# Performance work log

Measured on AMD Instinct MI355X. Metric: run time of the kernel, lower is better.

Reference implementation:

```python
import jax, jax.numpy as jnp
import numpy as np


def _knn_idx(query, ref, k):
    # query [B,Q,F], ref [B,M,F] -> indices [B,Q,k] of k nearest refs (L2)
    d2 = (jnp.sum(query * query, -1)[..., None]
          - 2.0 * jnp.einsum('bqf,bmf->bqm', query, ref)
          + jnp.sum(ref * ref, -1)[:, None, :])
    _, idx = jax.lax.top_k(-d2, k)
    return idx


def _gather(pts, idx):
    # pts [B,M,F], idx [B,Q,k] -> [B,Q,k,F]
    return jax.vmap(lambda p, i: p[i])(pts, idx)


def _mlp(h, W1, b1, W2, b2):
    # pointwise 1x1-conv MLP: Conv1d(k=1) == per-point matmul
    return jax.nn.relu(h @ W1 + b1) @ W2 + b2


def setup_inputs() -> dict:
    key = jax.random.key(0)
    ks = jax.random.split(key, 12)
    B, N, S1, S2 = 8, 16384, 512, 128

    def p(k, shape, fan):
        return jax.random.normal(k, shape, jnp.float32) / np.float32(np.sqrt(fan))

    return {
        'x': jax.random.normal(ks[0], (B, N, 3), jnp.float32),
        'sample_idx1': jnp.sort(jax.random.randint(ks[1], (S1,), 0, N)),
        'sample_idx2': jnp.sort(jax.random.randint(ks[2], (S2,), 0, S1)),
        'sa1_W1': p(ks[3], (3, 64), 3), 'sa1_b1': jnp.zeros((64,), jnp.float32),
        'sa1_W2': p(ks[4], (64, 64), 64), 'sa1_b2': jnp.zeros((64,), jnp.float32),
        'sa2_W1': p(ks[5], (64, 128), 64), 'sa2_b1': jnp.zeros((128,), jnp.float32),
        'sa2_W2': p(ks[6], (128, 128), 128), 'sa2_b2': jnp.zeros((128,), jnp.float32),
        'fp1_W1': p(ks[7], (192, 64), 192), 'fp1_b1': jnp.zeros((64,), jnp.float32),
        'fp1_W2': p(ks[8], (64, 64), 64), 'fp1_b2': jnp.zeros((64,), jnp.float32),
        'fp2_W1': p(ks[9], (67, 32), 67), 'fp2_b1': jnp.zeros((32,), jnp.float32),
        'fp2_W2': p(ks[10], (32, 32), 32), 'fp2_b2': jnp.zeros((32,), jnp.float32),
        'fc_W': p(ks[11], (32, 2), 32), 'fc_b': jnp.zeros((2,), jnp.float32),
    }


def reference(x, sample_idx1, sample_idx2,
              sa1_W1, sa1_b1, sa1_W2, sa1_b2,
              sa2_W1, sa2_b1, sa2_W2, sa2_b2,
              fp1_W1, fp1_b1, fp1_W2, fp1_b2,
              fp2_W1, fp2_b1, fp2_W2, fp2_b2,
              fc_W, fc_b):
    G = 32  # group_points
    # --- SetAbstraction 1 (KNN grouping in xyz space) ---
    samp1 = x[:, sample_idx1]                                  # [B,S1,3]
    g1 = _gather(x, _knn_idx(samp1, x, G))                     # [B,S1,G,3]
    feat1 = jnp.max(_mlp(g1, sa1_W1, sa1_b1, sa1_W2, sa1_b2), axis=2)   # [B,S1,64]
    # --- SetAbstraction 2 (point cloud = SA1 features, as in source) ---
    samp2 = feat1[:, sample_idx2]                              # [B,S2,64]
    g2 = _gather(feat1, _knn_idx(samp2, feat1, G))             # [B,S2,G,64]
    feat2 = jnp.max(_mlp(g2, sa2_W1, sa2_b1, sa2_W2, sa2_b2), axis=2)   # [B,S2,128]
    coords2 = samp1[:, sample_idx2]                            # [B,S2,3]
    # --- FeaturePropagation 1: interpolate feat2 onto the S1 points (3-NN mean) ---
    interp1 = jnp.mean(_gather(feat2, _knn_idx(samp1, coords2, 3)), axis=2)  # [B,S1,128]
    h1 = _mlp(jnp.concatenate([feat1, interp1], -1), fp1_W1, fp1_b1, fp1_W2, fp1_b2)  # [B,S1,64]
    # --- FeaturePropagation 2: interpolate onto all N points ---
    interp2 = jnp.mean(_gather(h1, _knn_idx(x, samp1, 3)), axis=2)           # [B,N,64]
    h2 = _mlp(jnp.concatenate([x, interp2], -1), fp2_W1, fp2_b1, fp2_W2, fp2_b2)      # [B,N,32]
    return jax.nn.sigmoid(h2 @ fc_W + fc_b)                    # [B,N,2]
```

## Files before the change

### kernel.cpp

```cpp
#include <hip/hip_runtime.h>
#include <hip/hip_bf16.h>

#define NB   8
#define NPTS 16384
#define NS1  512
#define NS2  128
#define KNN  32
#define FINF 3.402823466e+38f
#define NINF_BITS ((int)0xFF800000)

__device__ __forceinline__ void topk32f(float key, int idx, int lane,
                                        float& lkey, int& lidx, float& tau,
                                        unsigned long long mask) {
  const bool is16 = (lane == 16);
  while (mask) {
    const int src = (int)(__ffsll((long long)mask) - 1);
    mask &= mask - 1;
    const float ck = __int_as_float(
        __builtin_amdgcn_readlane(__float_as_int(key), src));
    if (ck < tau) {
      const int ci = __builtin_amdgcn_readlane(idx, src);
      const int upk0 = __builtin_amdgcn_update_dpp(
          NINF_BITS, __float_as_int(lkey), 0x111, 0xf, 0xf, false);
      const int upi0 = __builtin_amdgcn_update_dpp(
          0, lidx, 0x111, 0xf, 0xf, false);
      const int pk = __builtin_amdgcn_readlane(__float_as_int(lkey), 15);
      const int pi = __builtin_amdgcn_readlane(lidx, 15);
      const float up  = __int_as_float(is16 ? pk : upk0);
      const int   upi = is16 ? pi : upi0;
      const bool keep  = (lkey <= ck);
      const bool useup = (up > ck);
      const float nk = keep ? lkey : (useup ? up : ck);
      const int   ni = keep ? lidx : (useup ? upi : ci);
      if (lane < 32) { lkey = nk; lidx = ni; }
      tau = __int_as_float(__builtin_amdgcn_readlane(__float_as_int(lkey), 31));
    }
  }
}

__device__ __forceinline__ void merge3(float& d0, int& j0, float& d1, int& j1,
                                       float& d2, int& j2, int xm) {
  float e0 = __shfl_xor(d0, xm), e1 = __shfl_xor(d1, xm), e2 = __shfl_xor(d2, xm);
  int   f0 = __shfl_xor(j0, xm), f1 = __shfl_xor(j1, xm), f2 = __shfl_xor(j2, xm);
  float a0 = d0, a1 = d1, a2 = d2;
  int   b0 = j0, b1 = j1, b2 = j2;
  float od0, od1, od2; int oj0, oj1, oj2;
  #pragma unroll
  for (int r = 0; r < 3; ++r) {
    bool ta = (a0 < e0) || (a0 == e0 && b0 < f0);
    float sd = ta ? a0 : e0; int sj = ta ? b0 : f0;
    a0 = ta ? a1 : a0;  b0 = ta ? b1 : b0;
    a1 = ta ? a2 : a1;  b1 = ta ? b2 : b1;
    a2 = ta ? FINF : a2;
    e0 = ta ? e0 : e1;  f0 = ta ? f0 : f1;
    e1 = ta ? e1 : e2;  f1 = ta ? f1 : f2;
    e2 = ta ? e2 : FINF;
    if (r == 0) { od0 = sd; oj0 = sj; }
    else if (r == 1) { od1 = sd; oj1 = sj; }
    else { od2 = sd; oj2 = sj; }
  }
  d0 = od0; j0 = oj0; d1 = od1; j1 = oj1; d2 = od2; j2 = oj2;
}

extern "C" __global__ void __launch_bounds__(256)
prep_kernel(const float* __restrict__ x, float4* __restrict__ xr) {
  const int i = blockIdx.x * 256 + threadIdx.x;
  const float rx = x[i*3+0], ry = x[i*3+1], rz = x[i*3+2];
  xr[i] = make_float4(rx, ry, rz, rx*rx + ry*ry + rz*rz);
}

#define PROCF(rr, jbase)                                                      \
  {                                                                           \
    const float d = (Q.w - 2.0f*(Q.x*rr.x + Q.y*rr.y + Q.z*rr.z)) + rr.w;     \
    const unsigned long long mask = __ballot(d < tau);                        \
    if (mask) topk32f(d, (jbase) + lane, lane, lkey, lidx, tau, mask);        \
  }

extern "C" __global__ void __launch_bounds__(256)
knn1_kernel(const float4* __restrict__ xr, const int* __restrict__ sidx1,
            int* __restrict__ idx1) {
  const int w = threadIdx.x >> 6, lane = threadIdx.x & 63;
  const int gq = blockIdx.x * 4 + w;
  const int b = gq >> 9, q = gq & (NS1 - 1);
  const float4* xb = xr + (size_t)b * NPTS;
  const float4 Q = xb[sidx1[q]];
  float lkey = FINF, tau = FINF;
  int lidx = 0;
  float4 r0 = xb[0*64+lane], r1 = xb[1*64+lane], r2 = xb[2*64+lane], r3 = xb[3*64+lane];
  float4 r4 = xb[4*64+lane], r5 = xb[5*64+lane], r6 = xb[6*64+lane], r7 = xb[7*64+lane];
  for (int t = 0; t < 256; t += 8) {
    PROCF(r0, (t+0)*64);  r0 = xb[((t+ 8)&255)*64 + lane];
    PROCF(r1, (t+1)*64);  r1 = xb[((t+ 9)&255)*64 + lane];
    PROCF(r2, (t+2)*64);  r2 = xb[((t+10)&255)*64 + lane];
    PROCF(r3, (t+3)*64);  r3 = xb[((t+11)&255)*64 + lane];
    PROCF(r4, (t+4)*64);  r4 = xb[((t+12)&255)*64 + lane];
    PROCF(r5, (t+5)*64);  r5 = xb[((t+13)&255)*64 + lane];
    PROCF(r6, (t+6)*64);  r6 = xb[((t+14)&255)*64 + lane];
    PROCF(r7, (t+7)*64);  r7 = xb[((t+15)&255)*64 + lane];
  }
  if (lane < 32) idx1[gq*KNN + lane] = lidx;
}

extern "C" __global__ void __launch_bounds__(256)
mlp1_kernel(const float* __restrict__ x, const int* __restrict__ sidx1,
            const int* __restrict__ idx1,
            const float* __restrict__ W1, const float* __restrict__ b1,
            const float* __restrict__ W2, const float* __restrict__ b2,
            float* __restrict__ feat1, float* __restrict__ rr1,
            float* __restrict__ samp1) {
  __shared__ float P[32][3];
  __shared__ float H[32][64];
  __shared__ float PM[4][64];
  const int tid = threadIdx.x;
  const int gq = blockIdx.x;
  const int b = gq >> 9, q = gq & (NS1-1);
  const float* xb = x + (size_t)b * NPTS * 3;
  const int* nb = idx1 + gq * KNN;
  if (tid < 96) { int n = tid/3, d = tid - n*3; P[n][d] = xb[nb[n]*3 + d]; }
  __syncthreads();
  #pragma unroll
  for (int i = 0; i < 8; ++i) {
    int e = tid + 256*i, n = e >> 6, c = e & 63;
    float h = b1[c] + P[n][0]*W1[c] + P[n][1]*W1[64+c] + P[n][2]*W1[128+c];
    H[n][c] = fmaxf(h, 0.0f);
  }
  __syncthreads();
  const int g = tid >> 6, c = tid & 63;
  float acc[8];
  #pragma unroll
  for (int k = 0; k < 8; ++k) acc[k] = 0.0f;
  for (int j = 0; j < 64; j += 4) {
    float w0 = W2[j*64+c], w1 = W2[(j+1)*64+c], w2 = W2[(j+2)*64+c], w3 = W2[(j+3)*64+c];
    #pragma unroll
    for (int k = 0; k < 8; ++k) {
      float4 h4 = *(const float4*)&H[g*8+k][j];
      acc[k] = fmaf(h4.w, w3, fmaf(h4.z, w2, fmaf(h4.y, w1, fmaf(h4.x, w0, acc[k]))));
    }
  }
  float m = acc[0];
  #pragma unroll
  for (int k = 1; k < 8; ++k) m = fmaxf(m, acc[k]);
  PM[g][c] = m;
  __syncthreads();
  if (tid < 64) {
    float v = fmaxf(fmaxf(PM[0][tid], PM[1][tid]), fmaxf(PM[2][tid], PM[3][tid])) + b2[tid];
    feat1[(size_t)gq*64 + tid] = v;
    float s = v*v;
    #pragma unroll
    for (int off = 32; off; off >>= 1) s += __shfl_xor(s, off);
    if (tid == 0) rr1[gq] = s;
  } else if (tid < 67) {
    int d = tid - 64;
    samp1[(size_t)gq*3 + d] = xb[sidx1[q]*3 + d];
  }
}

extern "C" __global__ void __launch_bounds__(256)
knn2_kernel(const float* __restrict__ feat1, const float* __restrict__ rr1,
            const int* __restrict__ sidx2, int* __restrict__ idx2) {
  __shared__ float qrow[4][64];
  const int w = threadIdx.x >> 6, lane = threadIdx.x & 63;
  const int gq = blockIdx.x*4 + w;
  const int b = gq >> 7, q = gq & (NS2-1);
  const int sq = sidx2[q];
  const float* f1b = feat1 + (size_t)b * NS1 * 64;
  const float* rrb = rr1 + b * NS1;
  qrow[w][lane] = f1b[sq*64 + lane];
  __syncthreads();
  const float qq = rrb[sq];
  float lkey = FINF, tau = FINF;
  int lidx = 0;
  for (int t = 0; t < NS1/64; ++t) {
    const int j = t*64 + lane;
    const float* rrow = f1b + j*64;
    float dot = 0.0f;
    #pragma unroll
    for (int f = 0; f < 64; f += 4) {
      float4 r4 = *(const float4*)(rrow + f);
      dot = fmaf(qrow[w][f+3], r4.w, fmaf(qrow[w][f+2], r4.z,
            fmaf(qrow[w][f+1], r4.y, fmaf(qrow[w][f+0], r4.x, dot))));
    }
    const float d = (qq - 2.0f*dot) + rrb[j];
    const unsigned long long mask = __ballot(d < tau);
    if (mask) topk32f(d, j, lane, lkey, lidx, tau, mask);
  }
  if (lane < 32) idx2[gq*KNN + lane] = lidx;
}

extern "C" __global__ void __launch_bounds__(256)
mlp2_kernel(const float* __restrict__ feat1, const int* __restrict__ idx2,
            const float* __restrict__ W1, const float* __restrict__ b1,
            const float* __restrict__ W2, const float* __restrict__ b2,
            float* __restrict__ feat2) {
  __shared__ float Gm[32][64];
  __shared__ float H[32][128];
  __shared__ float PM[2][128];
  const int tid = threadIdx.x;
  const int gq = blockIdx.x;
  const int b = gq >> 7;
  const float* f1b = feat1 + (size_t)b * NS1 * 64;
  const int* nb = idx2 + gq * KNN;
  #pragma unroll
  for (int i = 0; i < 8; ++i) {
    int e = tid + 256*i, n = e >> 6, f = e & 63;
    Gm[n][f] = f1b[nb[n]*64 + f];
  }
  __syncthreads();
  #pragma unroll
  for (int i = 0; i < 16; ++i) {
    int e = tid + 256*i, n = e >> 7, c = e & 127;
    float h = b1[c];
    for (int f = 0; f < 64; f += 4) {
      float4 g4 = *(const float4*)&Gm[n][f];
      h = fmaf(g4.x, W1[f*128+c], h);
      h = fmaf(g4.y, W1[(f+1)*128+c], h);
      h = fmaf(g4.z, W1[(f+2)*128+c], h);
      h = fmaf(g4.w, W1[(f+3)*128+c], h);
    }
    H[n][c] = fmaxf(h, 0.0f);
  }
  __syncthreads();
  const int g = tid >> 7, c = tid & 127;
  float acc[16];
  #pragma unroll
  for (int k = 0; k < 16; ++k) acc[k] = 0.0f;
  for (int j = 0; j < 128; j += 4) {
    float w0 = W2[j*128+c], w1 = W2[(j+1)*128+c], w2 = W2[(j+2)*128+c], w3 = W2[(j+3)*128+c];
    #pragma unroll
    for (int k = 0; k < 16; ++k) {
      float4 h4 = *(const float4*)&H[g*16+k][j];
      acc[k] = fmaf(h4.w, w3, fmaf(h4.z, w2, fmaf(h4.y, w1, fmaf(h4.x, w0, acc[k]))));
    }
  }
  float m = acc[0];
  #pragma unroll
  for (int k = 1; k < 16; ++k) m = fmaxf(m, acc[k]);
  PM[g][c] = m;
  __syncthreads();
  if (tid < 128) feat2[(size_t)gq*128 + tid] = fmaxf(PM[0][tid], PM[1][tid]) + b2[tid];
}

extern "C" __global__ void __launch_bounds__(256)
fp1_kernel(const float* __restrict__ samp1, const int* __restrict__ sidx2,
           const float* __restrict__ feat1, const float* __restrict__ feat2,
           const float* __restrict__ W1, const float* __restrict__ b1,
           const float* __restrict__ W2, const float* __restrict__ b2,
           float* __restrict__ h1) {
  __shared__ float interp[4][128];
  __shared__ float hbuf[4][64];
  const int w = threadIdx.x >> 6, lane = threadIdx.x & 63;
  const int gq = blockIdx.x*4 + w;
  const int b = gq >> 9, q = gq & (NS1-1);
  const float* s1b = samp1 + (size_t)b * NS1 * 3;
  const float qx = s1b[q*3+0], qy = s1b[q*3+1], qz = s1b[q*3+2];
  const float qq = qx*qx + qy*qy + qz*qz;
  float d0, d1; int j0i, j1i;
  {
    const int rs = sidx2[lane];
    const float rx = s1b[rs*3+0], ry = s1b[rs*3+1], rz = s1b[rs*3+2];
    d0 = (qq - 2.0f*(qx*rx+qy*ry+qz*rz)) + (rx*rx+ry*ry+rz*rz);
    j0i = lane;
  }
  {
    const int j = lane + 64;
    const int rs = sidx2[j];
    const float rx = s1b[rs*3+0], ry = s1b[rs*3+1], rz = s1b[rs*3+2];
    d1 = (qq - 2.0f*(qx*rx+qy*ry+qz*rz)) + (rx*rx+ry*ry+rz*rz);
    j1i = j;
  }
  if (d1 < d0) { float td = d0; d0 = d1; d1 = td; int tj = j0i; j0i = j1i; j1i = tj; }
  float dA = d0, dB = d1, dC = FINF;
  int   jA = j0i, jB = j1i, jC = 0;
  merge3(dA, jA, dB, jB, dC, jC, 1);
  merge3(dA, jA, dB, jB, dC, jC, 2);
  merge3(dA, jA, dB, jB, dC, jC, 4);
  merge3(dA, jA, dB, jB, dC, jC, 8);
  merge3(dA, jA, dB, jB, dC, jC, 16);
  merge3(dA, jA, dB, jB, dC, jC, 32);
  const int r0 = jA, r1 = jB, r2 = jC;
  const float* f2b = feat2 + (size_t)b * NS2 * 128;
  interp[w][lane] =
      (f2b[r0*128+lane] + f2b[r1*128+lane] + f2b[r2*128+lane]) * (1.0f/3.0f);
  interp[w][lane+64] =
      (f2b[r0*128+64+lane] + f2b[r1*128+64+lane] + f2b[r2*128+64+lane]) * (1.0f/3.0f);
  __syncthreads();
  const float* f1row = feat1 + (size_t)gq * 64;
  float h = b1[lane];
  for (int f = 0; f < 64; ++f)  h = fmaf(f1row[f], W1[f*64+lane], h);
  for (int f = 0; f < 128; ++f) h = fmaf(interp[w][f], W1[(64+f)*64+lane], h);
  hbuf[w][lane] = fmaxf(h, 0.0f);
  __syncthreads();
  float o = b2[lane];
  for (int f = 0; f < 64; ++f) o = fmaf(hbuf[w][f], W2[f*64+lane], o);
  h1[(size_t)gq*64 + lane] = o;
}

extern "C" __global__ void __launch_bounds__(256, 4)
fp2a_kernel(const float* __restrict__ x, const float* __restrict__ samp1,
            ushort4* __restrict__ knn3) {
  __shared__ float4 RS[NS1];
  const int tid = threadIdx.x;
  const int b = blockIdx.x >> 8;
  const int pbase = (blockIdx.x & 255) * 64;
  for (int e = tid; e < NS1; e += 256) {
    const float rx = samp1[((size_t)b*NS1 + e)*3 + 0];
    const float ry = samp1[((size_t)b*NS1 + e)*3 + 1];
    const float rz = samp1[((size_t)b*NS1 + e)*3 + 2];
    RS[e] = make_float4(rx, ry, rz, rx*rx + ry*ry + rz*rz);
  }
  __syncthreads();
  const int p = pbase + (tid >> 2);
  const int q4 = tid & 3;
  const float* xb = x + (size_t)b * NPTS * 3;
  const float qx = xb[p*3+0], qy = xb[p*3+1], qz = xb[p*3+2];
  const float qq = qx*qx + qy*qy + qz*qz;
  float d0 = FINF, d1 = FINF, d2 = FINF;
  int j0 = 0, j1 = 0, j2 = 0;
  const float4* RQ = RS + q4*128;
  #pragma unroll 4
  for (int i = 0; i < 128; ++i) {
    const float4 r = RQ[i];
    const float dot = qx*r.x + qy*r.y + qz*r.z;
    const float d = (qq - 2.0f*dot) + r.w;
    const int j = q4*128 + i;
    const bool c2 = d < d2, c1 = d < d1, c0 = d < d0;
    d2 = c1 ? d1 : (c2 ? d : d2);  j2 = c1 ? j1 : (c2 ? j : j2);
    d1 = c0 ? d0 : (c1 ? d : d1);  j1 = c0 ? j0 : (c1 ? j : j1);
    d0 = c0 ? d : d0;              j0 = c0 ? j : j0;
  }
  merge3(d0, j0, d1, j1, d2, j2, 1);
  merge3(d0, j0, d1, j1, d2, j2, 2);
  if (q4 == 0) {
    ushort4 o;
    o.x = (unsigned short)j0; o.y = (unsigned short)j1;
    o.z = (unsigned short)j2; o.w = 0;
    knn3[(size_t)b*NPTS + p] = o;
  }
}

extern "C" __global__ void __launch_bounds__(256, 4)
fp2b_kernel(const float* __restrict__ x, const ushort4* __restrict__ knn3,
            const float* __restrict__ h1,
            const float* __restrict__ W1, const float* __restrict__ b1,
            const float* __restrict__ W2, const float* __restrict__ b2,
            const float* __restrict__ fcW, const float* __restrict__ fcb,
            float* __restrict__ out) {
  __shared__ float Xe[64][68];
  __shared__ float W1s[67*32];
  __shared__ float Hs[64][36];
  __shared__ ushort4 kid[64];
  __shared__ float WcS[64];
  __shared__ float bcS[2];
  const int tid = threadIdx.x;
  const int b = blockIdx.x >> 8;
  const int pbase = (blockIdx.x & 255) * 64;
  const float* xb = x + (size_t)b * NPTS * 3;
  const float* h1b = h1 + (size_t)b * NS1 * 64;
  if (tid < 64) {
    kid[tid] = knn3[(size_t)b*NPTS + pbase + tid];
    Xe[tid][0] = xb[(pbase+tid)*3+0];
    Xe[tid][1] = xb[(pbase+tid)*3+1];
    Xe[tid][2] = xb[(pbase+tid)*3+2];
  }
  for (int e = tid; e < 67*32; e += 256) W1s[e] = W1[e];
  __syncthreads();
  {
    const int sub = tid >> 6, f = tid & 63;
    #pragma unroll 4
    for (int i = 0; i < 16; ++i) {
      const int p = i*4 + sub;
      const ushort4 kk = kid[p];
      const float v = (h1b[(int)kk.x*64 + f] + h1b[(int)kk.y*64 + f] +
                       h1b[(int)kk.z*64 + f]) * (1.0f/3.0f);
      Xe[p][3+f] = v;
    }
  }
  __syncthreads();
  if (tid < 64) {
    const int k = tid >> 1, col = tid & 1;
    float s = 0.0f;
    for (int c = 0; c < 32; ++c) s = fmaf(W2[k*32+c], fcW[c*2+col], s);
    WcS[k*2+col] = s;
  } else if (tid < 66) {
    const int col = tid & 1;
    float s = fcb[col];
    for (int c = 0; c < 32; ++c) s = fmaf(b2[c], fcW[c*2+col], s);
    bcS[col] = s;
  }
  {
    const int p = tid >> 2, c0 = (tid & 3) * 8;
    float acc[8];
    const float4 bb0 = *(const float4*)(b1 + c0);
    const float4 bb1 = *(const float4*)(b1 + c0 + 4);
    acc[0]=bb0.x; acc[1]=bb0.y; acc[2]=bb0.z; acc[3]=bb0.w;
    acc[4]=bb1.x; acc[5]=bb1.y; acc[6]=bb1.z; acc[7]=bb1.w;
    for (int f = 0; f < 67; ++f) {
      const float xv = Xe[p][f];
      const float4 w0 = *(const float4*)&W1s[f*32 + c0];
      const float4 w1 = *(const float4*)&W1s[f*32 + c0 + 4];
      acc[0] = fmaf(xv, w0.x, acc[0]);
      acc[1] = fmaf(xv, w0.y, acc[1]);
      acc[2] = fmaf(xv, w0.z, acc[2]);
      acc[3] = fmaf(xv, w0.w, acc[3]);
      acc[4] = fmaf(xv, w1.x, acc[4]);
      acc[5] = fmaf(xv, w1.y, acc[5]);
      acc[6] = fmaf(xv, w1.z, acc[6]);
      acc[7] = fmaf(xv, w1.w, acc[7]);
    }
    *(float4*)&Hs[p][c0]   = make_float4(fmaxf(acc[0],0.f), fmaxf(acc[1],0.f),
                                         fmaxf(acc[2],0.f), fmaxf(acc[3],0.f));
    *(float4*)&Hs[p][c0+4] = make_float4(fmaxf(acc[4],0.f), fmaxf(acc[5],0.f),
                                         fmaxf(acc[6],0.f), fmaxf(acc[7],0.f));
  }
  __syncthreads();
  if (tid < 128) {
    const int p = tid >> 1, col = tid & 1;
    float s = bcS[col];
    for (int c = 0; c < 32; ++c) s = fmaf(Hs[p][c], WcS[c*2+col], s);
    out[((size_t)b*NPTS + pbase + p)*2 + col] = 1.0f / (1.0f + expf(-s));
  }
}

extern "C" void kernel_launch(void* const* d_in, const int* in_sizes, int n_in,
                              void* d_out, int out_size, void* d_ws, size_t ws_size,
                              hipStream_t stream) {
  const float* x     = (const float*)d_in[0];
  const int*   sidx1 = (const int*)d_in[1];
  const int*   sidx2 = (const int*)d_in[2];
  const float* sa1W1 = (const float*)d_in[3];
  const float* sa1b1 = (const float*)d_in[4];
  const float* sa1W2 = (const float*)d_in[5];
  const float* sa1b2 = (const float*)d_in[6];
  const float* sa2W1 = (const float*)d_in[7];
  const float* sa2b1 = (const float*)d_in[8];
  const float* sa2W2 = (const float*)d_in[9];
  const float* sa2b2 = (const float*)d_in[10];
  const float* fp1W1 = (const float*)d_in[11];
  const float* fp1b1 = (const float*)d_in[12];
  const float* fp1W2 = (const float*)d_in[13];
  const float* fp1b2 = (const float*)d_in[14];
  const float* fp2W1 = (const float*)d_in[15];
  const float* fp2b1 = (const float*)d_in[16];
  const float* fp2W2 = (const float*)d_in[17];
  const float* fp2b2 = (const float*)d_in[18];
  const float* fcW   = (const float*)d_in[19];
  const float* fcb   = (const float*)d_in[20];
  float* out = (float*)d_out;

  char* ws = (char*)d_ws;
  float4* xr   = (float4*)(ws + 0);
  float* feat1 = (float*)(ws + 0);
  float* rr1   = (float*)(ws + 1048576);
  float* samp1 = (float*)(ws + 1064960);
  float* feat2 = (float*)(ws + 1114112);
  float* h1    = (float*)(ws + 1638400);
  int*   idx1  = (int*)  (ws + 2686976);
  int*   idx2  = (int*)  (ws + 3211264);
  ushort4* knn3 = (ushort4*)(ws + 0);

  hipLaunchKernelGGL(prep_kernel, dim3(512), dim3(256), 0, stream, x, xr);
  hipLaunchKernelGGL(knn1_kernel, dim3(1024), dim3(256), 0, stream,
                     xr, sidx1, idx1);
  hipLaunchKernelGGL(mlp1_kernel, dim3(4096), dim3(256), 0, stream,
                     x, sidx1, idx1, sa1W1, sa1b1, sa1W2, sa1b2,
                     feat1, rr1, samp1);
  hipLaunchKernelGGL(knn2_kernel, dim3(256), dim3(256), 0, stream,
                     feat1, rr1, sidx2, idx2);
  hipLaunchKernelGGL(mlp2_kernel, dim3(1024), dim3(256), 0, stream,
                     feat1, idx2, sa2W1, sa2b1, sa2W2, sa2b2, feat2);
  hipLaunchKernelGGL(fp1_kernel, dim3(1024), dim3(256), 0, stream,
                     samp1, sidx2, feat1, feat2, fp1W1, fp1b1, fp1W2, fp1b2, h1);
  hipLaunchKernelGGL(fp2a_kernel, dim3(2048), dim3(256), 0, stream,
                     x, samp1, knn3);
  hipLaunchKernelGGL(fp2b_kernel, dim3(2048), dim3(256), 0, stream,
                     x, knn3, h1, fp2W1, fp2b1, fp2W2, fp2b2, fcW, fcb, out);
}
```

Measured before the change: 256.6 us.

## Fuse knn2 into mlp2 and fp2a into fp2b, keeping neighbor indices in LDS

Merges the SA2 KNN search into the SA2 MLP kernel. Each block now handles one query, with four wavefronts each scanning 128 candidates and then merging their partial top-32 lists in LDS. The FP2 3-NN search is folded into the final MLP kernel, so neighbor indices stay in shared memory instead of passing through global memory. This removes two launches and the global index round-trips, at the cost of more LDS per block, lower occupancy (launch bounds drop from 4 to 3), and an extra serial merge step run by a single wave.

```diff
diff --git a/kernel.cpp b/kernel.cpp
--- a/kernel.cpp
+++ b/kernel.cpp
@@ -156,54 +156,61 @@
 }
 
 extern "C" __global__ void __launch_bounds__(256)
-knn2_kernel(const float* __restrict__ feat1, const float* __restrict__ rr1,
-            const int* __restrict__ sidx2, int* __restrict__ idx2) {
-  __shared__ float qrow[4][64];
-  const int w = threadIdx.x >> 6, lane = threadIdx.x & 63;
-  const int gq = blockIdx.x*4 + w;
+knn2mlp2_kernel(const float* __restrict__ feat1, const float* __restrict__ rr1,
+                const int* __restrict__ sidx2,
+                const float* __restrict__ W1, const float* __restrict__ b1,
+                const float* __restrict__ W2, const float* __restrict__ b2,
+                float* __restrict__ feat2) {
+  __shared__ float qrow[64];
+  __shared__ float SK[4][32];
+  __shared__ int   SI[4][32];
+  __shared__ int   NBs[32];
+  __shared__ float Gm[32][64];
+  __shared__ float H[32][128];
+  __shared__ float PM[2][128];
+  const int tid = threadIdx.x, w = tid >> 6, lane = tid & 63;
+  const int gq = blockIdx.x;
   const int b = gq >> 7, q = gq & (NS2-1);
-  const int sq = sidx2[q];
   const float* f1b = feat1 + (size_t)b * NS1 * 64;
   const float* rrb = rr1 + b * NS1;
-  qrow[w][lane] = f1b[sq*64 + lane];
+  const int sq = sidx2[q];
+  if (tid < 64) qrow[tid] = f1b[sq*64 + tid];
   __syncthreads();
   const float qq = rrb[sq];
   float lkey = FINF, tau = FINF;
   int lidx = 0;
-  for (int t = 0; t < NS1/64; ++t) {
-    const int j = t*64 + lane;
+  #pragma unroll
+  for (int t = 0; t < 2; ++t) {
+    const int j = w*128 + t*64 + lane;
     const float* rrow = f1b + j*64;
     float dot = 0.0f;
     #pragma unroll
     for (int f = 0; f < 64; f += 4) {
       float4 r4 = *(const float4*)(rrow + f);
-      dot = fmaf(qrow[w][f+3], r4.w, fmaf(qrow[w][f+2], r4.z,
-            fmaf(qrow[w][f+1], r4.y, fmaf(qrow[w][f+0], r4.x, dot))));
+      dot = fmaf(qrow[f+3], r4.w, fmaf(qrow[f+2], r4.z,
+            fmaf(qrow[f+1], r4.y, fmaf(qrow[f+0], r4.x, dot))));
     }
     const float d = (qq - 2.0f*dot) + rrb[j];
     const unsigned long long mask = __ballot(d < tau);
     if (mask) topk32f(d, j, lane, lkey, lidx, tau, mask);
   }
-  if (lane < 32) idx2[gq*KNN + lane] = lidx;
-}
-
-extern "C" __global__ void __launch_bounds__(256)
-mlp2_kernel(const float* __restrict__ feat1, const int* __restrict__ idx2,
-            const float* __restrict__ W1, const float* __restrict__ b1,
-            const float* __restrict__ W2, const float* __restrict__ b2,
-            float* __restrict__ feat2) {
-  __shared__ float Gm[32][64];
-  __shared__ float H[32][128];
-  __shared__ float PM[2][128];
-  const int tid = threadIdx.x;
-  const int gq = blockIdx.x;
-  const int b = gq >> 7;
-  const float* f1b = feat1 + (size_t)b * NS1 * 64;
-  const int* nb = idx2 + gq * KNN;
+  if (lane < 32) { SK[w][lane] = lkey; SI[w][lane] = lidx; }
+  __syncthreads();
+  if (w == 0) {
+    #pragma unroll
+    for (int ww = 1; ww < 4; ++ww) {
+      const float mk = (lane < 32) ? SK[ww][lane] : FINF;
+      const int   mi = (lane < 32) ? SI[ww][lane] : 0;
+      const unsigned long long mmask = __ballot(mk < tau);
+      if (mmask) topk32f(mk, mi, lane, lkey, lidx, tau, mmask);
+    }
+    if (lane < 32) NBs[lane] = lidx;
+  }
+  __syncthreads();
   #pragma unroll
   for (int i = 0; i < 8; ++i) {
     int e = tid + 256*i, n = e >> 6, f = e & 63;
-    Gm[n][f] = f1b[nb[n]*64 + f];
+    Gm[n][f] = f1b[NBs[n]*64 + f];
   }
   __syncthreads();
   #pragma unroll
@@ -295,60 +302,18 @@
   h1[(size_t)gq*64 + lane] = o;
 }
 
-extern "C" __global__ void __launch_bounds__(256, 4)
-fp2a_kernel(const float* __restrict__ x, const float* __restrict__ samp1,
-            ushort4* __restrict__ knn3) {
+extern "C" __global__ void __launch_bounds__(256, 3)
+fp2_kernel(const float* __restrict__ x, const float* __restrict__ samp1,
+           const float* __restrict__ h1,
+           const float* __restrict__ W1, const float* __restrict__ b1,
+           const float* __restrict__ W2, const float* __restrict__ b2,
+           const float* __restrict__ fcW, const float* __restrict__ fcb,
+           float* __restrict__ out) {
   __shared__ float4 RS[NS1];
-  const int tid = threadIdx.x;
-  const int b = blockIdx.x >> 8;
-  const int pbase = (blockIdx.x & 255) * 64;
-  for (int e = tid; e < NS1; e += 256) {
-    const float rx = samp1[((size_t)b*NS1 + e)*3 + 0];
-    const float ry = samp1[((size_t)b*NS1 + e)*3 + 1];
-    const float rz = samp1[((size_t)b*NS1 + e)*3 + 2];
-    RS[e] = make_float4(rx, ry, rz, rx*rx + ry*ry + rz*rz);
-  }
-  __syncthreads();
-  const int p = pbase + (tid >> 2);
-  const int q4 = tid & 3;
-  const float* xb = x + (size_t)b * NPTS * 3;
-  const float qx = xb[p*3+0], qy = xb[p*3+1], qz = xb[p*3+2];
-  const float qq = qx*qx + qy*qy + qz*qz;
-  float d0 = FINF, d1 = FINF, d2 = FINF;
-  int j0 = 0, j1 = 0, j2 = 0;
-  const float4* RQ = RS + q4*128;
-  #pragma unroll 4
-  for (int i = 0; i < 128; ++i) {
-    const float4 r = RQ[i];
-    const float dot = qx*r.x + qy*r.y + qz*r.z;
-    const float d = (qq - 2.0f*dot) + r.w;
-    const int j = q4*128 + i;
-    const bool c2 = d < d2, c1 = d < d1, c0 = d < d0;
-    d2 = c1 ? d1 : (c2 ? d : d2);  j2 = c1 ? j1 : (c2 ? j : j2);
-    d1 = c0 ? d0 : (c1 ? d : d1);  j1 = c0 ? j0 : (c1 ? j : j1);
-    d0 = c0 ? d : d0;              j0 = c0 ? j : j0;
-  }
-  merge3(d0, j0, d1, j1, d2, j2, 1);
-  merge3(d0, j0, d1, j1, d2, j2, 2);
-  if (q4 == 0) {
-    ushort4 o;
-    o.x = (unsigned short)j0; o.y = (unsigned short)j1;
-    o.z = (unsigned short)j2; o.w = 0;
-    knn3[(size_t)b*NPTS + p] = o;
-  }
-}
-
-extern "C" __global__ void __launch_bounds__(256, 4)
-fp2b_kernel(const float* __restrict__ x, const ushort4* __restrict__ knn3,
-            const float* __restrict__ h1,
-            const float* __restrict__ W1, const float* __restrict__ b1,
-            const float* __restrict__ W2, const float* __restrict__ b2,
-            const float* __restrict__ fcW, const float* __restrict__ fcb,
-            float* __restrict__ out) {
+  __shared__ ushort4 kid[64];
   __shared__ float Xe[64][68];
   __shared__ float W1s[67*32];
   __shared__ float Hs[64][36];
-  __shared__ ushort4 kid[64];
   __shared__ float WcS[64];
   __shared__ float bcS[2];
   const int tid = threadIdx.x;
@@ -356,13 +321,46 @@
   const int pbase = (blockIdx.x & 255) * 64;
   const float* xb = x + (size_t)b * NPTS * 3;
   const float* h1b = h1 + (size_t)b * NS1 * 64;
+  for (int e = tid; e < NS1; e += 256) {
+    const float rx = samp1[((size_t)b*NS1 + e)*3 + 0];
+    const float ry = samp1[((size_t)b*NS1 + e)*3 + 1];
+    const float rz = samp1[((size_t)b*NS1 + e)*3 + 2];
+    RS[e] = make_float4(rx, ry, rz, rx*rx + ry*ry + rz*rz);
+  }
+  for (int e = tid; e < 67*32; e += 256) W1s[e] = W1[e];
   if (tid < 64) {
-    kid[tid] = knn3[(size_t)b*NPTS + pbase + tid];
     Xe[tid][0] = xb[(pbase+tid)*3+0];
     Xe[tid][1] = xb[(pbase+tid)*3+1];
     Xe[tid][2] = xb[(pbase+tid)*3+2];
   }
-  for (int e = tid; e < 67*32; e += 256) W1s[e] = W1[e];
+  __syncthreads();
+  {
+    const int pl = tid >> 2, q4 = tid & 3;
+    const float qx = Xe[pl][0], qy = Xe[pl][1], qz = Xe[pl][2];
+    const float qq = qx*qx + qy*qy + qz*qz;
+    float d0 = FINF, d1 = FINF, d2 = FINF;
+    int j0 = 0, j1 = 0, j2 = 0;
+    const float4* RQ = RS + q4*128;
+    #pragma unroll 4
+    for (int i = 0; i < 128; ++i) {
+      const float4 r = RQ[i];
+      const float dot = qx*r.x + qy*r.y + qz*r.z;
+      const float d = (qq - 2.0f*dot) + r.w;
+      const int j = q4*128 + i;
+      const bool c2 = d < d2, c1 = d < d1, c0 = d < d0;
+      d2 = c1 ? d1 : (c2 ? d : d2);  j2 = c1 ? j1 : (c2 ? j : j2);
+      d1 = c0 ? d0 : (c1 ? d : d1);  j1 = c0 ? j0 : (c1 ? j : j1);
+      d0 = c0 ? d : d0;              j0 = c0 ? j : j0;
+    }
+    merge3(d0, j0, d1, j1, d2, j2, 1);
+    merge3(d0, j0, d1, j1, d2, j2, 2);
+    if (q4 == 0) {
+      ushort4 o;
+      o.x = (unsigned short)j0; o.y = (unsigned short)j1;
+      o.z = (unsigned short)j2; o.w = 0;
+      kid[pl] = o;
+    }
+  }
   __syncthreads();
   {
     const int sub = tid >> 6, f = tid & 63;
@@ -455,8 +453,6 @@
   float* feat2 = (float*)(ws + 1114112);
   float* h1    = (float*)(ws + 1638400);
   int*   idx1  = (int*)  (ws + 2686976);
-  int*   idx2  = (int*)  (ws + 3211264);
-  ushort4* knn3 = (ushort4*)(ws + 0);
 
   hipLaunchKernelGGL(prep_kernel, dim3(512), dim3(256), 0, stream, x, xr);
   hipLaunchKernelGGL(knn1_kernel, dim3(1024), dim3(256), 0, stream,
@@ -464,14 +460,10 @@
   hipLaunchKernelGGL(mlp1_kernel, dim3(4096), dim3(256), 0, stream,
                      x, sidx1, idx1, sa1W1, sa1b1, sa1W2, sa1b2,
                      feat1, rr1, samp1);
-  hipLaunchKernelGGL(knn2_kernel, dim3(256), dim3(256), 0, stream,
-                     feat1, rr1, sidx2, idx2);
-  hipLaunchKernelGGL(mlp2_kernel, dim3(1024), dim3(256), 0, stream,
-                     feat1, idx2, sa2W1, sa2b1, sa2W2, sa2b2, feat2);
+  hipLaunchKernelGGL(knn2mlp2_kernel, dim3(1024), dim3(256), 0, stream,
+                     feat1, rr1, sidx2, sa2W1, sa2b1, sa2W2, sa2b2, feat2);
   hipLaunchKernelGGL(fp1_kernel, dim3(1024), dim3(256), 0, stream,
                      samp1, sidx2, feat1, feat2, fp1W1, fp1b1, fp1W2, fp1b2, h1);
-  hipLaunchKernelGGL(fp2a_kernel, dim3(2048), dim3(256), 0, stream,
-                     x, samp1, knn3);
-  hipLaunchKernelGGL(fp2b_kernel, dim3(2048), dim3(256), 0, stream,
-                     x, knn3, h1, fp2W1, fp2b1, fp2W2, fp2b2, fcW, fcb, out);
-}
+  hipLaunchKernelGGL(fp2_kernel, dim3(2048), dim3(256), 0, stream,
+                     x, samp1, h1, fp2W1, fp2b1, fp2W2, fp2b2, fcW, fcb, out);
+}
```

After: 245.1 us. 4.5% less time.
